# Performance work log

Hardware: AMD Instinct MI355X
Metric: run time of the kernel (lower is better)

## Reference

```python
import jax, jax.numpy as jnp
import numpy as np

B, K, N = 8192, 4096, 4096
GROUP = 128
G = K // GROUP
NLEVELS = 16


def setup_inputs() -> dict:
    key = jax.random.key(0)
    k1, k2, k3, k4, k5 = jax.random.split(key, 5)
    x = jax.random.normal(k1, (B, K), dtype=jnp.float32)
    indices = jax.random.randint(k2, (N, K), 0, NLEVELS, dtype=jnp.int32)
    codebook = jax.random.normal(k3, (NLEVELS,), dtype=jnp.float32)
    weight_norms = jax.random.uniform(k4, (N, G), dtype=jnp.float32)
    # per-group orthogonal rotation matrices (QR of Gaussian, as in rotation='qr')
    A = jax.random.normal(k5, (G, GROUP, GROUP), dtype=jnp.float32)
    Q, _ = jnp.linalg.qr(A)  # (G, GROUP, GROUP)
    return {"x": x, "indices": indices, "codebook": codebook,
            "weight_norms": weight_norms, "rotations": Q}


def reference(x, indices, codebook, weight_norms, rotations):
    """TurboQuantLinear forward (single pass, no bias, no residual).

    For each group g:
      x_rot_g = x[:, gs:ge] @ Pi_g.T
      out    += (x_rot_g @ codebook[idx_g].T) * (norms[:, g] / sqrt(group_size))
    Vectorized over groups.
    """
    b, k = x.shape
    g, gs, _ = rotations.shape
    n = indices.shape[0]
    scale = jnp.sqrt(jnp.asarray(gs, dtype=x.dtype))
    xg = x.reshape(b, g, gs)                                   # (B, G, gs)
    x_rot = jnp.einsum('bgk,gjk->bgj', xg, rotations)          # x_g @ Pi_g.T
    W = codebook[indices].reshape(n, g, gs)                    # dequant (N, G, gs)
    out = jnp.einsum('bgj,ngj,ng->bn', x_rot, W, weight_norms) / scale
    return out
```

## Files before the change

kernel.cpp:

```cpp
#include <hip/hip_runtime.h>
#include <hip/hip_bf16.h>

#define B_DIM 8192
#define K_DIM 4096
#define N_DIM 4096
#define GROUP 128
#define NG    (K_DIM / GROUP)
#define INV_SQRT_GROUP 0.08838834764831845f

using bf16x8 = __attribute__((ext_vector_type(8))) short;
using f32x4  = __attribute__((ext_vector_type(4))) float;

__device__ inline unsigned short f2bf(float f) {
    union { float f; unsigned u; } v; v.f = f;
    unsigned r = v.u + 0x7fffu + ((v.u >> 16) & 1u);
    return (unsigned short)(r >> 16);
}

#define GLOAD_LDS16(gp, lp)                                                   \
    __builtin_amdgcn_global_load_lds(                                         \
        (__attribute__((address_space(1))) void*)(gp),                        \
        (__attribute__((address_space(3))) void*)(lp), 16, 0, 0)

__global__ __launch_bounds__(256) void cast_x_kernel(
    const float* __restrict__ x, unsigned short* __restrict__ xb, size_t n8)
{
    size_t i = (size_t)blockIdx.x * blockDim.x + threadIdx.x;
    if (i >= n8) return;
    const float4* xp = (const float4*)x;
    float4 a = xp[2 * i];
    float4 b = xp[2 * i + 1];
    union { unsigned short s[8]; uint4 v; } pk;
    pk.s[0] = f2bf(a.x); pk.s[1] = f2bf(a.y); pk.s[2] = f2bf(a.z); pk.s[3] = f2bf(a.w);
    pk.s[4] = f2bf(b.x); pk.s[5] = f2bf(b.y); pk.s[6] = f2bf(b.z); pk.s[7] = f2bf(b.w);
    ((uint4*)xb)[i] = pk.v;
}

__global__ __launch_bounds__(256) void cast_rot_kernel(
    const float* __restrict__ rot, unsigned short* __restrict__ Rt)
{
    const int g = blockIdx.x;
    const float* Rg = rot + (size_t)g * GROUP * GROUP;
    unsigned short* Rtg = Rt + (size_t)g * GROUP * GROUP;
    for (int e = threadIdx.x; e < 128 * 32; e += 256) {
        int j = e >> 5, kc = (e & 31) * 4;
        float4 v = *(const float4*)(Rg + (size_t)j * 128 + kc);
        Rtg[(size_t)(kc + 0) * 128 + j] = f2bf(v.x);
        Rtg[(size_t)(kc + 1) * 128 + j] = f2bf(v.y);
        Rtg[(size_t)(kc + 2) * 128 + j] = f2bf(v.z);
        Rtg[(size_t)(kc + 3) * 128 + j] = f2bf(v.w);
    }
}

__global__ __launch_bounds__(256) void prep_v_kernel(
    const int*   __restrict__ indices,
    const float* __restrict__ codebook,
    const float* __restrict__ norms,
    const unsigned short* __restrict__ Rt,
    unsigned short* __restrict__ Vout)
{
    const int g  = blockIdx.y;
    const int n0 = blockIdx.x * 128;
    const int tid = threadIdx.x;

    __shared__ __attribute__((aligned(16))) unsigned short w_lds[128][136];
    __shared__ float s_lds[128];
    __shared__ float cb_lds[16];

    if (tid < 16)  cb_lds[tid] = codebook[tid];
    if (tid < 128) s_lds[tid] = norms[(size_t)(n0 + tid) * NG + g] * INV_SQRT_GROUP;
    __syncthreads();

    for (int e = tid; e < 128 * 16; e += 256) {
        const int nl = e >> 4, jc = e & 15;
        const float s = s_lds[nl];
        const int4* ip = (const int4*)(indices + (size_t)(n0 + nl) * K_DIM + g * GROUP + jc * 8);
        int4 i0 = ip[0];
        int4 i1 = ip[1];
        union { unsigned short h[8]; uint4 v; } pk;
        pk.h[0] = f2bf(cb_lds[i0.x] * s); pk.h[1] = f2bf(cb_lds[i0.y] * s);
        pk.h[2] = f2bf(cb_lds[i0.z] * s); pk.h[3] = f2bf(cb_lds[i0.w] * s);
        pk.h[4] = f2bf(cb_lds[i1.x] * s); pk.h[5] = f2bf(cb_lds[i1.y] * s);
        pk.h[6] = f2bf(cb_lds[i1.z] * s); pk.h[7] = f2bf(cb_lds[i1.w] * s);
        *(uint4*)&w_lds[nl][jc * 8] = pk.v;
    }
    __syncthreads();

    const int lane = tid & 63;
    const int wv   = tid >> 6;
    const int l15  = lane & 15;
    const int quad = lane >> 4;
    const int wn = (wv >> 1) * 64;
    const int wk = (wv & 1) * 64;

    const unsigned short* Rtg = Rt + (size_t)g * GROUP * GROUP;

    f32x4 acc[4][4] = {};

    for (int js = 0; js < 4; ++js) {
        const int jo = js * 32 + quad * 8;
        bf16x8 aF[4], bF[4];
        for (int mi = 0; mi < 4; ++mi)
            aF[mi] = *(const bf16x8*)&w_lds[wn + mi * 16 + l15][jo];
        for (int ni = 0; ni < 4; ++ni) {
            const int k = wk + ni * 16 + l15;
            bF[ni] = *(const bf16x8*)(Rtg + (size_t)k * 128 + jo);
        }
        for (int mi = 0; mi < 4; ++mi)
            for (int ni = 0; ni < 4; ++ni)
                acc[mi][ni] = __builtin_amdgcn_mfma_f32_16x16x32_bf16(
                    aF[mi], bF[ni], acc[mi][ni], 0, 0, 0);
    }

    for (int mi = 0; mi < 4; ++mi) {
        int n = n0 + wn + mi * 16 + quad * 4;
        for (int ni = 0; ni < 4; ++ni) {
            int k = wk + ni * 16 + l15;
            unsigned short* dst = Vout + (size_t)n * K_DIM + g * GROUP + k;
            for (int r = 0; r < 4; ++r)
                dst[(size_t)r * K_DIM] = f2bf(acc[mi][ni][r]);
        }
    }
}

__global__ __launch_bounds__(256) void gemm_bt_kernel(
    const unsigned short* __restrict__ A,
    const unsigned short* __restrict__ Bm,
    float* __restrict__ C)
{
    const int tid = threadIdx.x;
    const int n0 = blockIdx.x * 128;
    const int m0 = blockIdx.y * 128;

    __shared__ __attribute__((aligned(16))) unsigned short a_lds[128 * 64];
    __shared__ __attribute__((aligned(16))) unsigned short b_lds[128 * 64];

    const int lane = tid & 63;
    const int wv   = tid >> 6;
    const int l15  = lane & 15;
    const int quad = lane >> 4;
    const int wm = (wv >> 1) * 64;
    const int wn = (wv & 1) * 64;

    int rr[4], ko[4], lb[4];
    for (int p = 0; p < 4; ++p) {
        int c = tid + 256 * p;
        rr[p] = c >> 3;
        ko[p] = ((c & 7) ^ (rr[p] & 7)) * 8;
        lb[p] = (tid & ~63) + 256 * p;
    }

    const int l7 = l15 & 7;
    const int koh0 = ((0 * 4 + quad) ^ l7) * 8;
    const int koh1 = ((1 * 4 + quad) ^ l7) * 8;

    f32x4 acc[4][4] = {};

    for (int kt = 0; kt < K_DIM / 64; ++kt) {
        const int k0 = kt * 64;
        for (int p = 0; p < 4; ++p) {
            GLOAD_LDS16(A  + (size_t)(m0 + rr[p]) * K_DIM + k0 + ko[p], a_lds + lb[p] * 8);
            GLOAD_LDS16(Bm + (size_t)(n0 + rr[p]) * K_DIM + k0 + ko[p], b_lds + lb[p] * 8);
        }
        __syncthreads();

        {
            bf16x8 aF[4], bF[4];
            for (int mi = 0; mi < 4; ++mi)
                aF[mi] = *(const bf16x8*)&a_lds[(wm + mi * 16 + l15) * 64 + koh0];
            for (int ni = 0; ni < 4; ++ni)
                bF[ni] = *(const bf16x8*)&b_lds[(wn + ni * 16 + l15) * 64 + koh0];
            for (int mi = 0; mi < 4; ++mi)
                for (int ni = 0; ni < 4; ++ni)
                    acc[mi][ni] = __builtin_amdgcn_mfma_f32_16x16x32_bf16(
                        aF[mi], bF[ni], acc[mi][ni], 0, 0, 0);
        }
        {
            bf16x8 aF[4], bF[4];
            for (int mi = 0; mi < 4; ++mi)
                aF[mi] = *(const bf16x8*)&a_lds[(wm + mi * 16 + l15) * 64 + koh1];
            for (int ni = 0; ni < 4; ++ni)
                bF[ni] = *(const bf16x8*)&b_lds[(wn + ni * 16 + l15) * 64 + koh1];
            for (int mi = 0; mi < 4; ++mi)
                for (int ni = 0; ni < 4; ++ni)
                    acc[mi][ni] = __builtin_amdgcn_mfma_f32_16x16x32_bf16(
                        aF[mi], bF[ni], acc[mi][ni], 0, 0, 0);
        }
        __syncthreads();
    }

    for (int mi = 0; mi < 4; ++mi) {
        int m = m0 + wm + mi * 16 + quad * 4;
        for (int ni = 0; ni < 4; ++ni) {
            int n = n0 + wn + ni * 16 + l15;
            float* dst = C + (size_t)m * N_DIM + n;
            for (int r = 0; r < 4; ++r)
                dst[(size_t)r * N_DIM] = acc[mi][ni][r];
        }
    }
}

extern "C" void kernel_launch(void* const* d_in, const int* in_sizes, int n_in,
                              void* d_out, int out_size, void* d_ws, size_t ws_size,
                              hipStream_t stream)
{
    const float* x        = (const float*)d_in[0];
    const int*   indices  = (const int*)d_in[1];
    const float* codebook = (const float*)d_in[2];
    const float* norms    = (const float*)d_in[3];
    const float* rot      = (const float*)d_in[4];
    float* out            = (float*)d_out;

    unsigned short* Rt = (unsigned short*)d_ws;
    unsigned short* Xb = Rt + (size_t)NG * GROUP * GROUP;
    unsigned short* V  = Xb + (size_t)B_DIM * K_DIM;

    {
        size_t n8 = (size_t)B_DIM * K_DIM / 8;
        cast_x_kernel<<<dim3((unsigned)(n8 / 256)), dim3(256), 0, stream>>>(x, Xb, n8);
        cast_rot_kernel<<<dim3(NG), dim3(256), 0, stream>>>(rot, Rt);
    }
    {
        dim3 grid(N_DIM / 128, NG);
        prep_v_kernel<<<grid, dim3(256), 0, stream>>>(indices, codebook, norms, Rt, V);
    }
    {
        dim3 grid(N_DIM / 128, B_DIM / 128);
        gemm_bt_kernel<<<grid, dim3(256), 0, stream>>>(Xb, V, out);
    }
}
```

Baseline: 655.4 us.

## Rewrite main GEMM as 256x256 tile, 8-wave, double-buffered pipelined kernel

```diff
diff --git a/kernel.cpp b/kernel.cpp
--- a/kernel.cpp
+++ b/kernel.cpp
@@ -21,6 +21,16 @@
     __builtin_amdgcn_global_load_lds(                                         \
         (__attribute__((address_space(1))) void*)(gp),                        \
         (__attribute__((address_space(3))) void*)(lp), 16, 0, 0)
+
+#define BAR()                                                                 \
+    {                                                                         \
+        asm volatile("" ::: "memory");                                        \
+        __builtin_amdgcn_s_barrier();                                         \
+        asm volatile("" ::: "memory");                                        \
+    }
+#define LGKM0()  asm volatile("s_waitcnt lgkmcnt(0)" ::: "memory")
+#define VMCNT(n) asm volatile("s_waitcnt vmcnt(" #n ")" ::: "memory")
+#define PRIO(p)  __builtin_amdgcn_s_setprio(p)
 
 __global__ __launch_bounds__(256) void cast_x_kernel(
     const float* __restrict__ x, unsigned short* __restrict__ xb, size_t n8)
@@ -123,81 +133,136 @@
     }
 }
 
-__global__ __launch_bounds__(256) void gemm_bt_kernel(
+template <int GRP, int NLO>
+__device__ __forceinline__ void mfma_quad(f32x4 (&acc)[8][4],
+                                          const bf16x8 (&aF)[4][2],
+                                          const bf16x8 (&bF)[4][2])
+{
+#pragma unroll
+    for (int mi = 0; mi < 4; ++mi)
+#pragma unroll
+        for (int nn = 0; nn < 2; ++nn)
+#pragma unroll
+            for (int kh = 0; kh < 2; ++kh)
+                acc[GRP * 4 + mi][NLO + nn] = __builtin_amdgcn_mfma_f32_16x16x32_bf16(
+                    aF[mi][kh], bF[NLO + nn][kh], acc[GRP * 4 + mi][NLO + nn], 0, 0, 0);
+}
+
+__global__ __launch_bounds__(512) void gemm256_kernel(
     const unsigned short* __restrict__ A,
     const unsigned short* __restrict__ Bm,
     float* __restrict__ C)
 {
     const int tid = threadIdx.x;
-    const int n0 = blockIdx.x * 128;
-    const int m0 = blockIdx.y * 128;
-
-    __shared__ __attribute__((aligned(16))) unsigned short a_lds[128 * 64];
-    __shared__ __attribute__((aligned(16))) unsigned short b_lds[128 * 64];
+    const int n0 = blockIdx.x * 256;
+    const int m0 = blockIdx.y * 256;
+
+    __shared__ __attribute__((aligned(16))) unsigned short a_lds[2 * 256 * 64];
+    __shared__ __attribute__((aligned(16))) unsigned short b_lds[2 * 256 * 64];
 
     const int lane = tid & 63;
     const int wv   = tid >> 6;
     const int l15  = lane & 15;
     const int quad = lane >> 4;
-    const int wm = (wv >> 1) * 64;
-    const int wn = (wv & 1) * 64;
+    const int wm   = wv >> 2;
+    const int wn   = wv & 3;
 
     int rr[4], ko[4], lb[4];
+#pragma unroll
     for (int p = 0; p < 4; ++p) {
-        int c = tid + 256 * p;
+        int c = tid + 512 * p;
         rr[p] = c >> 3;
-        ko[p] = ((c & 7) ^ (rr[p] & 7)) * 8;
-        lb[p] = (tid & ~63) + 256 * p;
-    }
-
-    const int l7 = l15 & 7;
-    const int koh0 = ((0 * 4 + quad) ^ l7) * 8;
-    const int koh1 = ((1 * 4 + quad) ^ l7) * 8;
-
-    f32x4 acc[4][4] = {};
-
-    for (int kt = 0; kt < K_DIM / 64; ++kt) {
-        const int k0 = kt * 64;
-        for (int p = 0; p < 4; ++p) {
-            GLOAD_LDS16(A  + (size_t)(m0 + rr[p]) * K_DIM + k0 + ko[p], a_lds + lb[p] * 8);
-            GLOAD_LDS16(Bm + (size_t)(n0 + rr[p]) * K_DIM + k0 + ko[p], b_lds + lb[p] * 8);
-        }
-        __syncthreads();
-
-        {
-            bf16x8 aF[4], bF[4];
-            for (int mi = 0; mi < 4; ++mi)
-                aF[mi] = *(const bf16x8*)&a_lds[(wm + mi * 16 + l15) * 64 + koh0];
-            for (int ni = 0; ni < 4; ++ni)
-                bF[ni] = *(const bf16x8*)&b_lds[(wn + ni * 16 + l15) * 64 + koh0];
-            for (int mi = 0; mi < 4; ++mi)
-                for (int ni = 0; ni < 4; ++ni)
-                    acc[mi][ni] = __builtin_amdgcn_mfma_f32_16x16x32_bf16(
-                        aF[mi], bF[ni], acc[mi][ni], 0, 0, 0);
-        }
-        {
-            bf16x8 aF[4], bF[4];
-            for (int mi = 0; mi < 4; ++mi)
-                aF[mi] = *(const bf16x8*)&a_lds[(wm + mi * 16 + l15) * 64 + koh1];
-            for (int ni = 0; ni < 4; ++ni)
-                bF[ni] = *(const bf16x8*)&b_lds[(wn + ni * 16 + l15) * 64 + koh1];
-            for (int mi = 0; mi < 4; ++mi)
-                for (int ni = 0; ni < 4; ++ni)
-                    acc[mi][ni] = __builtin_amdgcn_mfma_f32_16x16x32_bf16(
-                        aF[mi], bF[ni], acc[mi][ni], 0, 0, 0);
-        }
-        __syncthreads();
-    }
-
-    for (int mi = 0; mi < 4; ++mi) {
-        int m = m0 + wm + mi * 16 + quad * 4;
+        ko[p] = ((c & 7) ^ ((c >> 3) & 7)) * 8;
+        lb[p] = (tid & ~63) + 512 * p;
+    }
+
+    const int koh0 = ((0 * 4 + quad) ^ (l15 & 7)) * 8;
+    const int koh1 = ((1 * 4 + quad) ^ (l15 & 7)) * 8;
+    const int aBase = (wm * 128 + l15) * 64;
+    const int bBase = (wn * 64 + l15) * 64;
+
+    f32x4 acc[8][4] = {};
+    bf16x8 aF[4][2], bF[4][2];
+
+#define STAGE_A(bb, kt, p)                                                    \
+    GLOAD_LDS16(A + (size_t)(m0 + rr[p]) * K_DIM + (size_t)(kt) * 64 + ko[p], \
+                a_lds + (bb) * 16384 + lb[p] * 8)
+#define STAGE_B(bb, kt, p)                                                    \
+    GLOAD_LDS16(Bm + (size_t)(n0 + rr[p]) * K_DIM + (size_t)(kt) * 64 + ko[p],\
+                b_lds + (bb) * 16384 + lb[p] * 8)
+
+#pragma unroll
+    for (int p = 0; p < 4; ++p) STAGE_A(0, 0, p);
+#pragma unroll
+    for (int p = 0; p < 4; ++p) STAGE_B(0, 0, p);
+#pragma unroll
+    for (int p = 0; p < 4; ++p) STAGE_A(1, 1, p);
+    VMCNT(4);
+    BAR();
+
+    for (int t = 0; t < 64; ++t) {
+        const int b = t & 1;
+        const int boff = b * 16384;
+
+#pragma unroll
+        for (int mi = 0; mi < 4; ++mi) {
+            aF[mi][0] = *(const bf16x8*)&a_lds[boff + aBase + mi * 1024 + koh0];
+            aF[mi][1] = *(const bf16x8*)&a_lds[boff + aBase + mi * 1024 + koh1];
+        }
+#pragma unroll
+        for (int nn = 0; nn < 2; ++nn) {
+            bF[nn][0] = *(const bf16x8*)&b_lds[boff + bBase + nn * 1024 + koh0];
+            bF[nn][1] = *(const bf16x8*)&b_lds[boff + bBase + nn * 1024 + koh1];
+        }
+        if (t + 1 < 64) { STAGE_B(b ^ 1, t + 1, 0); STAGE_B(b ^ 1, t + 1, 1); }
+        BAR(); LGKM0();
+        PRIO(1); mfma_quad<0, 0>(acc, aF, bF); PRIO(0);
+        BAR();
+
+#pragma unroll
+        for (int nn = 2; nn < 4; ++nn) {
+            bF[nn][0] = *(const bf16x8*)&b_lds[boff + bBase + nn * 1024 + koh0];
+            bF[nn][1] = *(const bf16x8*)&b_lds[boff + bBase + nn * 1024 + koh1];
+        }
+        if (t + 1 < 64) { STAGE_B(b ^ 1, t + 1, 2); STAGE_B(b ^ 1, t + 1, 3); }
+        BAR(); LGKM0();
+        PRIO(1); mfma_quad<0, 2>(acc, aF, bF); PRIO(0);
+        BAR();
+
+#pragma unroll
+        for (int mi = 0; mi < 4; ++mi) {
+            aF[mi][0] = *(const bf16x8*)&a_lds[boff + aBase + 4096 + mi * 1024 + koh0];
+            aF[mi][1] = *(const bf16x8*)&a_lds[boff + aBase + 4096 + mi * 1024 + koh1];
+        }
+        BAR(); LGKM0();
+        PRIO(1); mfma_quad<1, 0>(acc, aF, bF); PRIO(0);
+        BAR();
+
+        if (t + 2 < 64) {
+#pragma unroll
+            for (int p = 0; p < 4; ++p) STAGE_A(b, t + 2, p);
+        }
+        BAR();
+        PRIO(1); mfma_quad<1, 2>(acc, aF, bF); PRIO(0);
+        if (t < 62)       { VMCNT(4); }
+        else if (t == 62) { VMCNT(0); }
+        BAR();
+    }
+
+#pragma unroll
+    for (int mi = 0; mi < 8; ++mi) {
+        int m = m0 + wm * 128 + mi * 16 + quad * 4;
+#pragma unroll
         for (int ni = 0; ni < 4; ++ni) {
-            int n = n0 + wn + ni * 16 + l15;
+            int n = n0 + wn * 64 + ni * 16 + l15;
             float* dst = C + (size_t)m * N_DIM + n;
+#pragma unroll
             for (int r = 0; r < 4; ++r)
                 dst[(size_t)r * N_DIM] = acc[mi][ni][r];
         }
     }
+#undef STAGE_A
+#undef STAGE_B
 }
 
 extern "C" void kernel_launch(void* const* d_in, const int* in_sizes, int n_in,
@@ -225,7 +290,7 @@
         prep_v_kernel<<<grid, dim3(256), 0, stream>>>(indices, codebook, norms, Rt, V);
     }
     {
-        dim3 grid(N_DIM / 128, B_DIM / 128);
-        gemm_bt_kernel<<<grid, dim3(256), 0, stream>>>(Xb, V, out);
-    }
-}
+        dim3 grid(N_DIM / 256, B_DIM / 256);
+        gemm256_kernel<<<grid, dim3(512), 0, stream>>>(Xb, V, out);
+    }
+}
```

Result: faster. 543.5 us (-17.1%).
